# Performance work log

Measured on AMD Instinct MI355X. Metric: run time of the kernel, lower is better.

The kernel has to match this reference:

```python
import jax, jax.numpy as jnp
import numpy as np

N = 8192      # nodes
F = 256       # in_features
H = 64        # hidden_dim
NEG = -9e15   # mask fill value from the torch source
EPS = 1e-5    # LayerNorm eps (torch default)


def setup_inputs() -> dict:
    key = jax.random.key(0)
    ks = jax.random.split(key, 6)
    x = jax.random.normal(ks[0], (N, F), jnp.float32)
    adj = jax.random.randint(ks[1], (N, N), 0, 2, jnp.int32)
    # Linear params (xavier-ish scale, zero bias as in reset_parameters)
    Wt = jax.random.normal(ks[2], (H, F), jnp.float32) * (1.0 / np.sqrt(F))
    bt = jnp.zeros((H,), jnp.float32)
    Wa = jax.random.normal(ks[3], (1, H), jnp.float32) * (1.0 / np.sqrt(H))
    ba = jnp.zeros((1,), jnp.float32)
    Wp = jax.random.normal(ks[4], (F, H), jnp.float32) * (1.0 / np.sqrt(H))
    bp = jnp.zeros((F,), jnp.float32)
    gamma = jnp.ones((F,), jnp.float32)
    beta = jnp.zeros((F,), jnp.float32)
    return dict(x=x, adj=adj, Wt=Wt, bt=bt, Wa=Wa, ba=ba,
                Wp=Wp, bp=bp, gamma=gamma, beta=beta)


def reference(x, adj, Wt, bt, Wa, ba, Wp, bp, gamma, beta):
    # h = feature_transform(x): [N, H]
    h = x @ Wt.T + bt
    # per-source-node scalar score, expanded over all N columns: [N, 1]
    s = jax.nn.leaky_relu(h @ Wa.T + ba, negative_slope=0.2)
    # adjacency-masked softmax over neighbors (dim=1); s broadcasts to [N, N]
    scores = jnp.where(adj > 0, s, jnp.float32(NEG))
    w = jax.nn.softmax(scores, axis=1)            # [N, N]
    # dropout inactive at inference -> identity
    neighbor = w @ h                               # [N, H]
    tf = neighbor @ Wp.T + bp                      # [N, F]
    # residual + LayerNorm
    y = x + tf
    mu = jnp.mean(y, axis=-1, keepdims=True)
    var = jnp.var(y, axis=-1, keepdims=True)
    return gamma * (y - mu) * jax.lax.rsqrt(var + EPS) + beta
```

## Files before the change

### kernel.cpp

```cpp
#include <hip/hip_runtime.h>
#include <stdint.h>

#define NN 8192
#define FF 256
#define HH 64

typedef __attribute__((ext_vector_type(8))) short bf16x8;
typedef __attribute__((ext_vector_type(4))) float f32x4;

__device__ __forceinline__ uint16_t f2bf(float f) {
  union { float f; uint32_t i; } c; c.f = f;
  uint32_t r = c.i + 0x7FFFu + ((c.i >> 16) & 1u);
  return (uint16_t)(r >> 16);
}

__global__ __launch_bounds__(256) void k1_h(
    const float* __restrict__ x, const float* __restrict__ Wt,
    const float* __restrict__ bt, uint16_t* __restrict__ hT) {
  __shared__ float wtT[256 * 65];
  __shared__ float sbt[64];
  __shared__ uint16_t s_tr[64][34];
  const int t = threadIdx.x;
  const int lane = t & 63;
  const int w = t >> 6;

  for (int i = 0; i < 64; ++i)
    wtT[t * 65 + i] = Wt[(size_t)i * FF + t];
  if (t < 64) sbt[t] = bt[t];
  __syncthreads();

  const int n0 = blockIdx.x * 32;
  const int r0 = n0 + w * 8;
  const float binit = sbt[lane];
  float acc[8];
#pragma unroll
  for (int r = 0; r < 8; ++r) acc[r] = binit;

  for (int f4 = 0; f4 < FF; f4 += 4) {
    float4 xs[8];
#pragma unroll
    for (int r = 0; r < 8; ++r)
      xs[r] = *(const float4*)(x + (size_t)(r0 + r) * FF + f4);
    const float wt0 = wtT[(f4 + 0) * 65 + lane];
    const float wt1 = wtT[(f4 + 1) * 65 + lane];
    const float wt2 = wtT[(f4 + 2) * 65 + lane];
    const float wt3 = wtT[(f4 + 3) * 65 + lane];
#pragma unroll
    for (int r = 0; r < 8; ++r)
      acc[r] += xs[r].x * wt0 + xs[r].y * wt1 + xs[r].z * wt2 + xs[r].w * wt3;
  }

#pragma unroll
  for (int r = 0; r < 8; ++r)
    s_tr[lane][w * 8 + r] = f2bf(acc[r]);
  __syncthreads();
#pragma unroll
  for (int i = 0; i < 4; ++i) {
    int idx = i * 256 + t;
    int c = idx >> 4;
    int d = idx & 15;
    uint32_t v = (uint32_t)s_tr[c][2 * d] | ((uint32_t)s_tr[c][2 * d + 1] << 16);
    *(uint32_t*)(hT + (size_t)c * NN + n0 + 2 * d) = v;
  }
}

__global__ __launch_bounds__(256) void k2_attn(
    const int* __restrict__ adj, const uint16_t* __restrict__ hT,
    float* __restrict__ nb_part, float* __restrict__ deg_part) {
  __shared__ __align__(16) unsigned char af[16 * 1024];
  __shared__ float s_part[4][16][64];
  __shared__ float s_degw[4][16];

  const int t    = threadIdx.x;
  const int w    = t >> 6;
  const int lane = t & 63;
  const int m    = lane & 15;
  const int q    = lane >> 4;
  const int g    = blockIdx.x >> 1;
  const int half = blockIdx.x & 1;
  const int row0 = g * 16;
  const int rsw  = (m & 7) << 4;

  bf16x8 vone;
#pragma unroll
  for (int j = 0; j < 8; ++j) vone[j] = (short)0x3F80;

  f32x4 acc0 = 0, acc1 = 0, acc2 = 0, acc3 = 0, accd = 0;
  const uint16_t* __restrict__ hrow = hT + (size_t)m * NN;
  const int sr = t >> 7;
  const int sc = t & 127;

  const int base = half * (NN / 2);
  for (int tile = 0; tile < 8; ++tile) {
    const int c0 = base + tile * 512;
#pragma unroll
    for (int i = 0; i < 8; ++i) {
      const int r_ = 2 * i + sr;
      int4 a = *(const int4*)(adj + (size_t)(row0 + r_) * NN + c0 + sc * 4);
      uint32_t lo = ((uint32_t)a.x | ((uint32_t)a.y << 16)) * 0x3F80u;
      uint32_t hi = ((uint32_t)a.z | ((uint32_t)a.w << 16)) * 0x3F80u;
      uint2 w2; w2.x = lo; w2.y = hi;
      *(uint2*)(af + r_ * 1024 + (((uint32_t)(sc * 8)) ^ ((r_ & 7) << 4))) = w2;
    }
    __syncthreads();
#pragma unroll
    for (int it = 0; it < 2; ++it) {
      const int kl = w * 128 + it * 64;
      const int k0 = c0 + kl + q * 8;
      const int k1 = k0 + 32;
      bf16x8 afA = *(const bf16x8*)(af + m * 1024 +
                                    (((uint32_t)((kl + q * 8) * 2)) ^ rsw));
      bf16x8 afB = *(const bf16x8*)(af + m * 1024 +
                                    (((uint32_t)((kl + q * 8) * 2 + 64)) ^ rsw));
      bf16x8 b0 = *(const bf16x8*)(hrow + k0);
      bf16x8 b1 = *(const bf16x8*)(hrow + 16 * NN + k0);
      bf16x8 b2 = *(const bf16x8*)(hrow + 32 * NN + k0);
      bf16x8 b3 = *(const bf16x8*)(hrow + 48 * NN + k0);
      bf16x8 d0 = *(const bf16x8*)(hrow + k1);
      bf16x8 d1 = *(const bf16x8*)(hrow + 16 * NN + k1);
      bf16x8 d2 = *(const bf16x8*)(hrow + 32 * NN + k1);
      bf16x8 d3 = *(const bf16x8*)(hrow + 48 * NN + k1);
      acc0 = __builtin_amdgcn_mfma_f32_16x16x32_bf16(afA, b0, acc0, 0, 0, 0);
      acc1 = __builtin_amdgcn_mfma_f32_16x16x32_bf16(afA, b1, acc1, 0, 0, 0);
      acc2 = __builtin_amdgcn_mfma_f32_16x16x32_bf16(afA, b2, acc2, 0, 0, 0);
      acc3 = __builtin_amdgcn_mfma_f32_16x16x32_bf16(afA, b3, acc3, 0, 0, 0);
      accd = __builtin_amdgcn_mfma_f32_16x16x32_bf16(afA, vone, accd, 0, 0, 0);
      acc0 = __builtin_amdgcn_mfma_f32_16x16x32_bf16(afB, d0, acc0, 0, 0, 0);
      acc1 = __builtin_amdgcn_mfma_f32_16x16x32_bf16(afB, d1, acc1, 0, 0, 0);
      acc2 = __builtin_amdgcn_mfma_f32_16x16x32_bf16(afB, d2, acc2, 0, 0, 0);
      acc3 = __builtin_amdgcn_mfma_f32_16x16x32_bf16(afB, d3, acc3, 0, 0, 0);
      accd = __builtin_amdgcn_mfma_f32_16x16x32_bf16(afB, vone, accd, 0, 0, 0);
    }
    __syncthreads();
  }

#pragma unroll
  for (int rg = 0; rg < 4; ++rg) {
    s_part[w][q * 4 + rg][ 0 + m] = acc0[rg];
    s_part[w][q * 4 + rg][16 + m] = acc1[rg];
    s_part[w][q * 4 + rg][32 + m] = acc2[rg];
    s_part[w][q * 4 + rg][48 + m] = acc3[rg];
  }
  if (m == 0) {
#pragma unroll
    for (int rg = 0; rg < 4; ++rg) s_degw[w][q * 4 + rg] = accd[rg];
  }
  __syncthreads();

  float* __restrict__ dst = nb_part + ((size_t)half * NN + row0) * HH;
  for (int idx = t; idx < 16 * 64; idx += 256) {
    int r = idx >> 6, c = idx & 63;
    float s = s_part[0][r][c] + s_part[1][r][c] +
              s_part[2][r][c] + s_part[3][r][c];
    dst[(size_t)r * HH + c] = s;
  }
  if (t < 16) {
    float d = s_degw[0][t] + s_degw[1][t] + s_degw[2][t] + s_degw[3][t];
    deg_part[half * NN + row0 + t] = d;
  }
}

__global__ __launch_bounds__(256) void k3_epi(
    const float* __restrict__ x, const float* __restrict__ nb_part,
    const float* __restrict__ deg_part, const float* __restrict__ Wp,
    const float* __restrict__ bp, const float* __restrict__ gamma,
    const float* __restrict__ beta, float* __restrict__ out) {
  __shared__ float s_nb[16][64];
  __shared__ float s_y[16 * 256];

  const int t    = threadIdx.x;
  const int w    = t >> 6;
  const int lane = t & 63;
  const int row0 = blockIdx.x * 16;

  for (int idx = t; idx < 16 * 64; idx += 256) {
    int r = idx >> 6, c = idx & 63;
    float d = deg_part[row0 + r] + deg_part[NN + row0 + r];
    float s = nb_part[(size_t)(row0 + r) * HH + c] +
              nb_part[(size_t)(NN + row0 + r) * HH + c];
    s_nb[r][c] = (d > 0.5f) ? s / d : 0.f;
  }
  __syncthreads();

  {
    const int f = t;
    float wp[64];
    const float* wrow = Wp + (size_t)f * HH;
#pragma unroll
    for (int j = 0; j < 16; ++j) {
      float4 v = *(const float4*)(wrow + j * 4);
      wp[j * 4 + 0] = v.x; wp[j * 4 + 1] = v.y;
      wp[j * 4 + 2] = v.z; wp[j * 4 + 3] = v.w;
    }
    const float bpf = bp[f];
    for (int r = 0; r < 16; ++r) {
      float a = bpf;
#pragma unroll
      for (int k = 0; k < 64; k += 4) {
        float4 nv = *(const float4*)&s_nb[r][k];
        a += nv.x * wp[k] + nv.y * wp[k + 1] + nv.z * wp[k + 2] + nv.w * wp[k + 3];
      }
      float y = x[(size_t)(row0 + r) * FF + f] + a;
      s_y[r * 256 + f] = y;
    }
  }
  __syncthreads();

  for (int i = 0; i < 4; ++i) {
    const int r = w * 4 + i;
    float4 v = *(const float4*)&s_y[r * 256 + lane * 4];
    float sum = v.x + v.y + v.z + v.w;
    float ss  = v.x * v.x + v.y * v.y + v.z * v.z + v.w * v.w;
#pragma unroll
    for (int o = 32; o >= 1; o >>= 1) {
      sum += __shfl_xor(sum, o, 64);
      ss  += __shfl_xor(ss, o, 64);
    }
    const float mu  = sum * (1.0f / 256.0f);
    const float var = ss * (1.0f / 256.0f) - mu * mu;
    const float rs  = rsqrtf(var + 1e-5f);
    const int f0 = lane * 4;
    float4 g = *(const float4*)(gamma + f0);
    float4 b = *(const float4*)(beta + f0);
    float4 o4;
    o4.x = g.x * (v.x - mu) * rs + b.x;
    o4.y = g.y * (v.y - mu) * rs + b.y;
    o4.z = g.z * (v.z - mu) * rs + b.z;
    o4.w = g.w * (v.w - mu) * rs + b.w;
    *(float4*)(out + (size_t)(row0 + r) * FF + f0) = o4;
  }
}

extern "C" void kernel_launch(void* const* d_in, const int* in_sizes, int n_in,
                              void* d_out, int out_size, void* d_ws, size_t ws_size,
                              hipStream_t stream) {
  const float* x     = (const float*)d_in[0];
  const int*   adj   = (const int*)d_in[1];
  const float* Wt    = (const float*)d_in[2];
  const float* bt    = (const float*)d_in[3];
  const float* Wp    = (const float*)d_in[6];
  const float* bp    = (const float*)d_in[7];
  const float* gamma = (const float*)d_in[8];
  const float* beta  = (const float*)d_in[9];
  float* out = (float*)d_out;

  uint16_t* hT       = (uint16_t*)d_ws;
  float*    nb_part  = (float*)((char*)d_ws + (1u << 20));
  float*    deg_part = (float*)((char*)d_ws + (5u << 20));

  k1_h   <<<256,  256, 0, stream>>>(x, Wt, bt, hT);
  k2_attn<<<1024, 256, 0, stream>>>(adj, hT, nb_part, deg_part);
  k3_epi <<<512,  256, 0, stream>>>(x, nb_part, deg_part, Wp, bp, gamma, beta, out);
}
```

Before: 436.7 us.

## Double-buffer adjacency tiles via direct global-to-LDS DMA loads

The adjacency staging in the attention kernel now uses global_load_lds to copy raw int32 adjacency straight into a double-buffered LDS tile, prefetching the next 256-column tile while the current one is consumed. The int-to-bf16 conversion moves from the staging step to the consumer side after the LDS read. This is meant to hide the latency of the dominant adjacency stream behind the MFMA work and cut register-staged copies. In exchange it doubles LDS use, which may lower occupancy, and it doubles the number of tiles and barriers.

```diff
diff --git a/kernel.cpp b/kernel.cpp
--- a/kernel.cpp
+++ b/kernel.cpp
@@ -12,6 +12,12 @@
   union { float f; uint32_t i; } c; c.f = f;
   uint32_t r = c.i + 0x7FFFu + ((c.i >> 16) & 1u);
   return (uint16_t)(r >> 16);
+}
+
+__device__ __forceinline__ void gload_lds16(const void* g, void* l) {
+  __builtin_amdgcn_global_load_lds(
+      (const __attribute__((address_space(1))) unsigned int*)g,
+      (__attribute__((address_space(3))) unsigned int*)l, 16, 0, 0);
 }
 
 __global__ __launch_bounds__(256) void k1_h(
@@ -67,7 +73,7 @@
 __global__ __launch_bounds__(256) void k2_attn(
     const int* __restrict__ adj, const uint16_t* __restrict__ hT,
     float* __restrict__ nb_part, float* __restrict__ deg_part) {
-  __shared__ __align__(16) unsigned char af[16 * 1024];
+  __shared__ __align__(16) unsigned char af[2][16384];
   __shared__ float s_part[4][16][64];
   __shared__ float s_degw[4][16];
 
@@ -79,7 +85,7 @@
   const int g    = blockIdx.x >> 1;
   const int half = blockIdx.x & 1;
   const int row0 = g * 16;
-  const int rsw  = (m & 7) << 4;
+  const uint32_t rsw = (uint32_t)((m & 7) << 4);
 
   bf16x8 vone;
 #pragma unroll
@@ -87,31 +93,49 @@
 
   f32x4 acc0 = 0, acc1 = 0, acc2 = 0, acc3 = 0, accd = 0;
   const uint16_t* __restrict__ hrow = hT + (size_t)m * NN;
-  const int sr = t >> 7;
-  const int sc = t & 127;
-
   const int base = half * (NN / 2);
-  for (int tile = 0; tile < 8; ++tile) {
-    const int c0 = base + tile * 512;
-#pragma unroll
-    for (int i = 0; i < 8; ++i) {
-      const int r_ = 2 * i + sr;
-      int4 a = *(const int4*)(adj + (size_t)(row0 + r_) * NN + c0 + sc * 4);
-      uint32_t lo = ((uint32_t)a.x | ((uint32_t)a.y << 16)) * 0x3F80u;
-      uint32_t hi = ((uint32_t)a.z | ((uint32_t)a.w << 16)) * 0x3F80u;
-      uint2 w2; w2.x = lo; w2.y = hi;
-      *(uint2*)(af + r_ * 1024 + (((uint32_t)(sc * 8)) ^ ((r_ & 7) << 4))) = w2;
-    }
-    __syncthreads();
-#pragma unroll
-    for (int it = 0; it < 2; ++it) {
-      const int kl = w * 128 + it * 64;
+
+  const int kl = w * 64;
+  const uint32_t cbA  = (uint32_t)((kl + q * 8) * 4);
+  const uint32_t o_a0 = (uint32_t)(m * 1024) + ( cbA         ^ rsw);
+  const uint32_t o_a1 = (uint32_t)(m * 1024) + ((cbA +  16u) ^ rsw);
+  const uint32_t o_b0 = (uint32_t)(m * 1024) + ((cbA + 128u) ^ rsw);
+  const uint32_t o_b1 = (uint32_t)(m * 1024) + ((cbA + 144u) ^ rsw);
+
+#define STAGE_DMA(BUF, C0)                                                   \
+  _Pragma("unroll") for (int j = 0; j < 4; ++j) {                            \
+    const int s_ = w * 4 + j;                                                \
+    gload_lds16(adj + (size_t)(row0 + s_) * NN + (C0) +                      \
+                    ((lane ^ (s_ & 7)) * 4),                                 \
+                &af[BUF][s_ * 1024]);                                        \
+  }
+
+  STAGE_DMA(0, base)
+  __syncthreads();
+
+  int c0 = base;
+  for (int tile = 0; tile < 16; ++tile) {
+    const int buf = tile & 1;
+    if (tile < 15) STAGE_DMA(buf ^ 1, c0 + 256)
+
+    {
+      const unsigned char* cb_ = af[buf];
+      int4 ra0 = *(const int4*)(cb_ + o_a0);
+      int4 ra1 = *(const int4*)(cb_ + o_a1);
+      int4 rb0 = *(const int4*)(cb_ + o_b0);
+      int4 rb1 = *(const int4*)(cb_ + o_b1);
+      union U { bf16x8 v; uint32_t u[4]; } afA, afB;
+      afA.u[0] = ((uint32_t)ra0.x | ((uint32_t)ra0.y << 16)) * 0x3F80u;
+      afA.u[1] = ((uint32_t)ra0.z | ((uint32_t)ra0.w << 16)) * 0x3F80u;
+      afA.u[2] = ((uint32_t)ra1.x | ((uint32_t)ra1.y << 16)) * 0x3F80u;
+      afA.u[3] = ((uint32_t)ra1.z | ((uint32_t)ra1.w << 16)) * 0x3F80u;
+      afB.u[0] = ((uint32_t)rb0.x | ((uint32_t)rb0.y << 16)) * 0x3F80u;
+      afB.u[1] = ((uint32_t)rb0.z | ((uint32_t)rb0.w << 16)) * 0x3F80u;
+      afB.u[2] = ((uint32_t)rb1.x | ((uint32_t)rb1.y << 16)) * 0x3F80u;
+      afB.u[3] = ((uint32_t)rb1.z | ((uint32_t)rb1.w << 16)) * 0x3F80u;
+
       const int k0 = c0 + kl + q * 8;
       const int k1 = k0 + 32;
-      bf16x8 afA = *(const bf16x8*)(af + m * 1024 +
-                                    (((uint32_t)((kl + q * 8) * 2)) ^ rsw));
-      bf16x8 afB = *(const bf16x8*)(af + m * 1024 +
-                                    (((uint32_t)((kl + q * 8) * 2 + 64)) ^ rsw));
       bf16x8 b0 = *(const bf16x8*)(hrow + k0);
       bf16x8 b1 = *(const bf16x8*)(hrow + 16 * NN + k0);
       bf16x8 b2 = *(const bf16x8*)(hrow + 32 * NN + k0);
@@ -120,19 +144,21 @@
       bf16x8 d1 = *(const bf16x8*)(hrow + 16 * NN + k1);
       bf16x8 d2 = *(const bf16x8*)(hrow + 32 * NN + k1);
       bf16x8 d3 = *(const bf16x8*)(hrow + 48 * NN + k1);
-      acc0 = __builtin_amdgcn_mfma_f32_16x16x32_bf16(afA, b0, acc0, 0, 0, 0);
-      acc1 = __builtin_amdgcn_mfma_f32_16x16x32_bf16(afA, b1, acc1, 0, 0, 0);
-      acc2 = __builtin_amdgcn_mfma_f32_16x16x32_bf16(afA, b2, acc2, 0, 0, 0);
-      acc3 = __builtin_amdgcn_mfma_f32_16x16x32_bf16(afA, b3, acc3, 0, 0, 0);
-      accd = __builtin_amdgcn_mfma_f32_16x16x32_bf16(afA, vone, accd, 0, 0, 0);
-      acc0 = __builtin_amdgcn_mfma_f32_16x16x32_bf16(afB, d0, acc0, 0, 0, 0);
-      acc1 = __builtin_amdgcn_mfma_f32_16x16x32_bf16(afB, d1, acc1, 0, 0, 0);
-      acc2 = __builtin_amdgcn_mfma_f32_16x16x32_bf16(afB, d2, acc2, 0, 0, 0);
-      acc3 = __builtin_amdgcn_mfma_f32_16x16x32_bf16(afB, d3, acc3, 0, 0, 0);
-      accd = __builtin_amdgcn_mfma_f32_16x16x32_bf16(afB, vone, accd, 0, 0, 0);
+      acc0 = __builtin_amdgcn_mfma_f32_16x16x32_bf16(afA.v, b0, acc0, 0, 0, 0);
+      acc1 = __builtin_amdgcn_mfma_f32_16x16x32_bf16(afA.v, b1, acc1, 0, 0, 0);
+      acc2 = __builtin_amdgcn_mfma_f32_16x16x32_bf16(afA.v, b2, acc2, 0, 0, 0);
+      acc3 = __builtin_amdgcn_mfma_f32_16x16x32_bf16(afA.v, b3, acc3, 0, 0, 0);
+      accd = __builtin_amdgcn_mfma_f32_16x16x32_bf16(afA.v, vone, accd, 0, 0, 0);
+      acc0 = __builtin_amdgcn_mfma_f32_16x16x32_bf16(afB.v, d0, acc0, 0, 0, 0);
+      acc1 = __builtin_amdgcn_mfma_f32_16x16x32_bf16(afB.v, d1, acc1, 0, 0, 0);
+      acc2 = __builtin_amdgcn_mfma_f32_16x16x32_bf16(afB.v, d2, acc2, 0, 0, 0);
+      acc3 = __builtin_amdgcn_mfma_f32_16x16x32_bf16(afB.v, d3, acc3, 0, 0, 0);
+      accd = __builtin_amdgcn_mfma_f32_16x16x32_bf16(afB.v, vone, accd, 0, 0, 0);
     }
     __syncthreads();
-  }
+    c0 += 256;
+  }
+#undef STAGE_DMA
 
 #pragma unroll
   for (int rg = 0; rg < 4; ++rg) {
```

Result: slower. 463.4 us (+6.1%).

## Pack adjacency into bitmask in pre-pass and expand bits in registers

Applied to the files above, without the earlier changes.

Adds a pre-pass kernel that reads the int32 adjacency matrix once and writes a 1-bit-per-edge mask through wave ballots. The attention kernel then reads 64-bit mask words per row and expands them directly into bf16 MFMA A-operands in registers. This removes the shared-memory staging buffer and both per-tile barriers from the attention loop, and adds a 4-wave occupancy hint. The full adjacency is still read once, so the cost moves into a streaming pack kernel plus an extra small mask round-trip and one more launch.

```diff
diff --git a/kernel.cpp b/kernel.cpp
--- a/kernel.cpp
+++ b/kernel.cpp
@@ -12,6 +12,18 @@
   union { float f; uint32_t i; } c; c.f = f;
   uint32_t r = c.i + 0x7FFFu + ((c.i >> 16) & 1u);
   return (uint16_t)(r >> 16);
+}
+
+__global__ __launch_bounds__(256) void k0_pack(
+    const int* __restrict__ adj, unsigned long long* __restrict__ maskp) {
+  const int lane = threadIdx.x & 63;
+  size_t idx = (size_t)blockIdx.x * 256 + threadIdx.x;
+  const size_t stride = (size_t)gridDim.x * 256;
+  for (; idx < (size_t)NN * NN; idx += stride) {
+    int v = adj[idx];
+    unsigned long long b = __ballot(v != 0);
+    if (lane == 0) maskp[idx >> 6] = b;
+  }
 }
 
 __global__ __launch_bounds__(256) void k1_h(
@@ -64,10 +76,10 @@
   }
 }
 
-__global__ __launch_bounds__(256) void k2_attn(
-    const int* __restrict__ adj, const uint16_t* __restrict__ hT,
+__global__ __launch_bounds__(256, 4) void k2_attn(
+    const unsigned long long* __restrict__ maskp,
+    const uint16_t* __restrict__ hT,
     float* __restrict__ nb_part, float* __restrict__ deg_part) {
-  __shared__ __align__(16) unsigned char af[16 * 1024];
   __shared__ float s_part[4][16][64];
   __shared__ float s_degw[4][16];
 
@@ -79,7 +91,6 @@
   const int g    = blockIdx.x >> 1;
   const int half = blockIdx.x & 1;
   const int row0 = g * 16;
-  const int rsw  = (m & 7) << 4;
 
   bf16x8 vone;
 #pragma unroll
@@ -87,31 +98,28 @@
 
   f32x4 acc0 = 0, acc1 = 0, acc2 = 0, acc3 = 0, accd = 0;
   const uint16_t* __restrict__ hrow = hT + (size_t)m * NN;
-  const int sr = t >> 7;
-  const int sc = t & 127;
-
+  const unsigned long long* __restrict__ mrow = maskp + (size_t)(row0 + m) * (NN / 64);
   const int base = half * (NN / 2);
+  const int qs = q * 8;
+
   for (int tile = 0; tile < 8; ++tile) {
     const int c0 = base + tile * 512;
 #pragma unroll
-    for (int i = 0; i < 8; ++i) {
-      const int r_ = 2 * i + sr;
-      int4 a = *(const int4*)(adj + (size_t)(row0 + r_) * NN + c0 + sc * 4);
-      uint32_t lo = ((uint32_t)a.x | ((uint32_t)a.y << 16)) * 0x3F80u;
-      uint32_t hi = ((uint32_t)a.z | ((uint32_t)a.w << 16)) * 0x3F80u;
-      uint2 w2; w2.x = lo; w2.y = hi;
-      *(uint2*)(af + r_ * 1024 + (((uint32_t)(sc * 8)) ^ ((r_ & 7) << 4))) = w2;
-    }
-    __syncthreads();
-#pragma unroll
     for (int it = 0; it < 2; ++it) {
       const int kl = w * 128 + it * 64;
-      const int k0 = c0 + kl + q * 8;
+      const int k0 = c0 + kl + qs;
       const int k1 = k0 + 32;
-      bf16x8 afA = *(const bf16x8*)(af + m * 1024 +
-                                    (((uint32_t)((kl + q * 8) * 2)) ^ rsw));
-      bf16x8 afB = *(const bf16x8*)(af + m * 1024 +
-                                    (((uint32_t)((kl + q * 8) * 2 + 64)) ^ rsw));
+      uint2 mw = *(const uint2*)(mrow + ((c0 + kl) >> 6));
+      uint32_t bA = (mw.x >> qs) & 0xFFu;
+      uint32_t bB = (mw.y >> qs) & 0xFFu;
+      union U { bf16x8 v; uint32_t u[4]; } afA, afB;
+#pragma unroll
+      for (int i = 0; i < 4; ++i) {
+        afA.u[i] = (((bA >> (2 * i)) & 1u) |
+                    (((bA >> (2 * i + 1)) & 1u) << 16)) * 0x3F80u;
+        afB.u[i] = (((bB >> (2 * i)) & 1u) |
+                    (((bB >> (2 * i + 1)) & 1u) << 16)) * 0x3F80u;
+      }
       bf16x8 b0 = *(const bf16x8*)(hrow + k0);
       bf16x8 b1 = *(const bf16x8*)(hrow + 16 * NN + k0);
       bf16x8 b2 = *(const bf16x8*)(hrow + 32 * NN + k0);
@@ -120,18 +128,17 @@
       bf16x8 d1 = *(const bf16x8*)(hrow + 16 * NN + k1);
       bf16x8 d2 = *(const bf16x8*)(hrow + 32 * NN + k1);
       bf16x8 d3 = *(const bf16x8*)(hrow + 48 * NN + k1);
-      acc0 = __builtin_amdgcn_mfma_f32_16x16x32_bf16(afA, b0, acc0, 0, 0, 0);
-      acc1 = __builtin_amdgcn_mfma_f32_16x16x32_bf16(afA, b1, acc1, 0, 0, 0);
-      acc2 = __builtin_amdgcn_mfma_f32_16x16x32_bf16(afA, b2, acc2, 0, 0, 0);
-      acc3 = __builtin_amdgcn_mfma_f32_16x16x32_bf16(afA, b3, acc3, 0, 0, 0);
-      accd = __builtin_amdgcn_mfma_f32_16x16x32_bf16(afA, vone, accd, 0, 0, 0);
-      acc0 = __builtin_amdgcn_mfma_f32_16x16x32_bf16(afB, d0, acc0, 0, 0, 0);
-      acc1 = __builtin_amdgcn_mfma_f32_16x16x32_bf16(afB, d1, acc1, 0, 0, 0);
-      acc2 = __builtin_amdgcn_mfma_f32_16x16x32_bf16(afB, d2, acc2, 0, 0, 0);
-      acc3 = __builtin_amdgcn_mfma_f32_16x16x32_bf16(afB, d3, acc3, 0, 0, 0);
-      accd = __builtin_amdgcn_mfma_f32_16x16x32_bf16(afB, vone, accd, 0, 0, 0);
-    }
-    __syncthreads();
+      acc0 = __builtin_amdgcn_mfma_f32_16x16x32_bf16(afA.v, b0, acc0, 0, 0, 0);
+      acc1 = __builtin_amdgcn_mfma_f32_16x16x32_bf16(afA.v, b1, acc1, 0, 0, 0);
+      acc2 = __builtin_amdgcn_mfma_f32_16x16x32_bf16(afA.v, b2, acc2, 0, 0, 0);
+      acc3 = __builtin_amdgcn_mfma_f32_16x16x32_bf16(afA.v, b3, acc3, 0, 0, 0);
+      accd = __builtin_amdgcn_mfma_f32_16x16x32_bf16(afA.v, vone, accd, 0, 0, 0);
+      acc0 = __builtin_amdgcn_mfma_f32_16x16x32_bf16(afB.v, d0, acc0, 0, 0, 0);
+      acc1 = __builtin_amdgcn_mfma_f32_16x16x32_bf16(afB.v, d1, acc1, 0, 0, 0);
+      acc2 = __builtin_amdgcn_mfma_f32_16x16x32_bf16(afB.v, d2, acc2, 0, 0, 0);
+      acc3 = __builtin_amdgcn_mfma_f32_16x16x32_bf16(afB.v, d3, acc3, 0, 0, 0);
+      accd = __builtin_amdgcn_mfma_f32_16x16x32_bf16(afB.v, vone, accd, 0, 0, 0);
+    }
   }
 
 #pragma unroll
@@ -244,11 +251,13 @@
   const float* beta  = (const float*)d_in[9];
   float* out = (float*)d_out;
 
-  uint16_t* hT       = (uint16_t*)d_ws;
-  float*    nb_part  = (float*)((char*)d_ws + (1u << 20));
-  float*    deg_part = (float*)((char*)d_ws + (5u << 20));
-
+  uint16_t*           hT       = (uint16_t*)d_ws;
+  float*              nb_part  = (float*)((char*)d_ws + (1u << 20));
+  float*              deg_part = (float*)((char*)d_ws + (5u << 20));
+  unsigned long long* maskp    = (unsigned long long*)((char*)d_ws + (6u << 20));
+
+  k0_pack<<<2048, 256, 0, stream>>>(adj, maskp);
   k1_h   <<<256,  256, 0, stream>>>(x, Wt, bt, hT);
-  k2_attn<<<1024, 256, 0, stream>>>(adj, hT, nb_part, deg_part);
+  k2_attn<<<1024, 256, 0, stream>>>(maskp, hT, nb_part, deg_part);
   k3_epi <<<512,  256, 0, stream>>>(x, nb_part, deg_part, Wp, bp, gamma, beta, out);
 }
```

After: 497.8 us. +14.0%, slower.
